# Kernel tuning notes

Measured on AMD Instinct MI355X. Metric: run time of the kernel, lower is better.

Reference implementation:

```python
import jax, jax.numpy as jnp
import numpy as np

D = 512      # input_size == per-head embed_size (wide attention)
H = 8        # num_attn_heads


def setup_inputs() -> dict:
    key = jax.random.key(0)
    ks = jax.random.split(key, 8)
    B, S = 2, 2048
    scale = 1.0 / np.sqrt(D)
    return {
        "Xin_q": jax.random.normal(ks[0], (B, S, D), dtype=jnp.float32),
        "Xin_k": jax.random.normal(ks[1], (B, S, D), dtype=jnp.float32),
        "Xin_v": jax.random.normal(ks[2], (B, S, D), dtype=jnp.float32),
        # per-head projection weights, stored as [H, D_in, D_out] (bias-free)
        "Wq": jax.random.normal(ks[3], (H, D, D), dtype=jnp.float32) * scale,
        "Wk": jax.random.normal(ks[4], (H, D, D), dtype=jnp.float32) * scale,
        "Wv": jax.random.normal(ks[5], (H, D, D), dtype=jnp.float32) * scale,
        # output projection: concat(H*D) -> D, with bias
        "Wz": jax.random.normal(ks[6], (H * D, D), dtype=jnp.float32) * (1.0 / np.sqrt(H * D)),
        "bz": jax.random.normal(ks[7], (D,), dtype=jnp.float32) * 0.01,
    }


def reference(Xin_q, Xin_k, Xin_v, Wq, Wk, Wv, Wz, bz):
    B, Sq, _ = Xin_q.shape
    inv4 = 1.0 / (D ** 0.25)  # each of Q and K scaled by embed_size**(1/4)
    # project all heads at once: [B,H,S,D]
    q = jnp.einsum("bsd,hde->bhse", Xin_q, Wq) * inv4
    k = jnp.einsum("bsd,hde->bhse", Xin_k, Wk) * inv4
    v = jnp.einsum("bsd,hde->bhse", Xin_v, Wv)
    attn = jax.nn.softmax(jnp.einsum("bhqe,bhke->bhqk", q, k), axis=-1)
    z = jnp.einsum("bhqk,bhke->bhqe", attn, v)        # [B,H,S,D]
    # concat heads along last dim (head-major order matches torch.cat over the head loop)
    z = jnp.transpose(z, (0, 2, 1, 3)).reshape(B, Sq, H * D)
    out = z @ Wz + bz                                  # [B,S,D]
    attn_avg = jnp.mean(attn, axis=1)                  # [B,Sq,Skv]
    return out, attn_avg
```

## Files before the change

### kernel.cpp

```cpp
#include <hip/hip_runtime.h>
#include <math.h>

#define BB 2
#define SS 2048
#define D_ 512
#define H_ 8
#define MS (BB * SS)
#define HD (H_ * D_)

typedef short bf16x8 __attribute__((ext_vector_type(8)));
typedef float f32x4 __attribute__((ext_vector_type(4)));

__device__ inline unsigned short f2bf(float f) {
    union { float f; unsigned u; } x{f};
    unsigned r = x.u + 0x7fff + ((x.u >> 16) & 1);
    return (unsigned short)(r >> 16);
}
__device__ inline float bf2f(unsigned short u) {
    union { unsigned u; float f; } x{(unsigned)u << 16};
    return x.f;
}

constexpr size_t SZ_X   = (size_t)MS * D_ * 2;
constexpr size_t SZ_W   = (size_t)H_ * D_ * D_ * 2;
constexpr size_t SZ_WZ  = (size_t)HD * D_ * 2;
constexpr size_t SZ_QK  = (size_t)H_ * MS * D_ * 2;
constexpr size_t SZ_SC  = (size_t)H_ * BB * SS * SS * 2;
constexpr size_t SZ_Z   = (size_t)MS * HD * 2;
constexpr size_t SZ_OP  = (size_t)2 * MS * D_ * 4;
constexpr size_t SZ_LV  = (size_t)H_ * BB * SS * 4;
constexpr size_t OFF_XQ  = 0;
constexpr size_t OFF_XK  = OFF_XQ + SZ_X;
constexpr size_t OFF_XV  = OFF_XK + SZ_X;
constexpr size_t OFF_WQT = OFF_XV + SZ_X;
constexpr size_t OFF_WKT = OFF_WQT + SZ_W;
constexpr size_t OFF_WVT = OFF_WKT + SZ_W;
constexpr size_t OFF_WZT = OFF_WVT + SZ_W;
constexpr size_t OFF_QB  = OFF_WZT + SZ_WZ;
constexpr size_t OFF_KB  = OFF_QB + SZ_QK;
constexpr size_t OFF_VT  = OFF_KB + SZ_QK;
constexpr size_t OFF_SC  = OFF_VT + SZ_QK;
constexpr size_t OFF_Z   = OFF_SC + SZ_SC;
constexpr size_t OFF_OP  = OFF_Z + SZ_Z;
constexpr size_t OFF_LV  = OFF_OP + SZ_OP;
constexpr size_t WS_TOTAL = OFF_LV + SZ_LV;
__device__ __align__(256) unsigned char g_ws[WS_TOTAL];

__device__ inline void gl2lds16(const unsigned short* g, unsigned short* l) {
    __builtin_amdgcn_global_load_lds(
        (const __attribute__((address_space(1))) void*)g,
        (__attribute__((address_space(3))) void*)l, 16, 0, 0);
}

#define BAR() __builtin_amdgcn_s_barrier()
#define PRIO1() __builtin_amdgcn_s_setprio(1)
#define PRIO0() __builtin_amdgcn_s_setprio(0)
#define VMW4() asm volatile("s_waitcnt vmcnt(4)" ::: "memory")
#define VMW0() asm volatile("s_waitcnt vmcnt(0)" ::: "memory")

__device__ __forceinline__ void rd_a(const unsigned short* p, int qm, int o0, int o1,
                                     bf16x8 (&Af)[8]) {
#pragma unroll
    for (int fi = 0; fi < 4; fi++) {
        Af[2 * fi]     = *(const bf16x8*)(p + (qm * 64 + fi * 16) * 64 + o0);
        Af[2 * fi + 1] = *(const bf16x8*)(p + (qm * 64 + fi * 16) * 64 + o1);
    }
}
__device__ __forceinline__ void rd_b(const unsigned short* p, int qn, int o0, int o1,
                                     bf16x8 (&Bf)[4]) {
#pragma unroll
    for (int fj = 0; fj < 2; fj++) {
        Bf[2 * fj]     = *(const bf16x8*)(p + (qn * 32 + fj * 16) * 64 + o0);
        Bf[2 * fj + 1] = *(const bf16x8*)(p + (qn * 32 + fj * 16) * 64 + o1);
    }
}
__device__ __forceinline__ void mma_q(int qm, int qn, const bf16x8 (&Af)[8],
                                      const bf16x8 (&Bf)[4], f32x4 (&acc)[8][4]) {
#pragma unroll
    for (int fi = 0; fi < 4; fi++)
#pragma unroll
        for (int fj = 0; fj < 2; fj++) {
            acc[qm * 4 + fi][qn * 2 + fj] = __builtin_amdgcn_mfma_f32_16x16x32_bf16(
                Af[2 * fi], Bf[2 * fj], acc[qm * 4 + fi][qn * 2 + fj], 0, 0, 0);
            acc[qm * 4 + fi][qn * 2 + fj] = __builtin_amdgcn_mfma_f32_16x16x32_bf16(
                Af[2 * fi + 1], Bf[2 * fj + 1], acc[qm * 4 + fi][qn * 2 + fj], 0, 0, 0);
        }
}

__global__ __launch_bounds__(512, 2) void gemm256_k(
    const unsigned short* __restrict__ A, const unsigned short* __restrict__ B,
    unsigned short* __restrict__ C, int K, int ldA, int ldB, int ldC,
    long sA1, long sA2, long sB1, long sB2, long sC1, long sC2, int d2,
    float alpha, int doExp, const float* __restrict__ rowScale, long sR1, long sR2,
    int gx, int gy, int gz)
{
    __shared__ unsigned short LA[2][256 * 64];
    __shared__ unsigned short LB[2][256 * 64];
    const int tid = threadIdx.x;
    const int w = tid >> 6, l = tid & 63;
    const int wm = w >> 2, wn = w & 3;

    const int sr = l >> 3;
    const int sq = (l & 7) ^ sr;
    const int q = l >> 4, sl = l & 7;
    const int o0 = (q ^ sl) * 8;
    const int o1 = ((q + 4) ^ sl) * 8;
    const unsigned short* pa0 = &LA[0][(wm * 128 + (l & 15)) * 64];
    const unsigned short* pa1 = &LA[1][(wm * 128 + (l & 15)) * 64];
    const unsigned short* pb0 = &LB[0][(wn * 64 + (l & 15)) * 64];
    const unsigned short* pb1 = &LB[1][(wn * 64 + (l & 15)) * 64];

    const int tilesPerZ = gx * gy;
    const int zPerXcd = gz >> 3;
    const int perXcd = zPerXcd * tilesPerZ;
    const int xcd = blockIdx.x & 7, jj = blockIdx.x >> 3;
    const int nT = (perXcd - jj + 31) >> 5;
    const int nK2 = K >> 7;

    auto decode = [&](int idx, const unsigned short*& gA, const unsigned short*& gB,
                      long& cO, long& rO, int& m0o, int& n0o) {
        const int zl = idx / tilesPerZ;
        const int rem = idx - zl * tilesPerZ;
        const int by = rem / gx;
        const int bx = rem - by * gx;
        const int bz = xcd * zPerXcd + zl;
        const int z1 = bz / d2, z2 = bz - z1 * d2;
        m0o = by * 256; n0o = bx * 256;
        gA = A + z1 * sA1 + z2 * sA2 + (long)(m0o + w * 16 + sr) * ldA + sq * 8;
        gB = B + z1 * sB1 + z2 * sB2 + (long)(n0o + w * 16 + sr) * ldB + sq * 8;
        cO = z1 * sC1 + z2 * sC2;
        rO = z1 * sR1 + z2 * sR2;
    };

    const unsigned short *gAc, *gBc, *gAn, *gBn;
    long cOff, rsOff, cOffN, rsOffN;
    int m0, n0, m0N, n0N;
    decode(jj, gAc, gBc, cOff, rsOff, m0, n0);
    gAn = gAc; gBn = gBc; cOffN = cOff; rsOffN = rsOff; m0N = m0; n0N = n0;

    f32x4 acc[8][4] = {};
    bf16x8 Af[8], Bf0[4], Bf1[4];

#define STG_A(bufi, half, base, t) do { \
    gl2lds16((base) + (long)((half) * 128) * ldA + (long)(t) * 64, \
             &LA[bufi][((half) * 128 + w * 16) * 64]); \
    gl2lds16((base) + (long)((half) * 128 + 8) * ldA + (long)(t) * 64, \
             &LA[bufi][((half) * 128 + w * 16 + 8) * 64]); } while (0)
#define STG_B(bufi, half, base, t) do { \
    gl2lds16((base) + (long)((half) * 128) * ldB + (long)(t) * 64, \
             &LB[bufi][((half) * 128 + w * 16) * 64]); \
    gl2lds16((base) + (long)((half) * 128 + 8) * ldB + (long)(t) * 64, \
             &LB[bufi][((half) * 128 + w * 16 + 8) * 64]); } while (0)

    STG_A(0, 0, gAc, 0); STG_A(0, 1, gAc, 0);
    STG_B(0, 0, gBc, 0); STG_B(0, 1, gBc, 0);
    STG_B(1, 0, gBc, 1); STG_B(1, 1, gBc, 1);
    VMW4();
    BAR();

    for (int k = 0; k < nT; ++k) {
        const bool hasNext = (k + 1 < nT);
        if (hasNext) decode(jj + (k + 1) * 32, gAn, gBn, cOffN, rsOffN, m0N, n0N);

        for (int u = 0; u < nK2; ++u) {
            const int t1 = 2 * u + 1, t2 = 2 * u + 2, t3 = 2 * u + 3;
            const bool lastU = (u == nK2 - 1);
            const bool stg = !lastU || hasNext;
            const unsigned short* a2 = lastU ? gAn : gAc;
            const unsigned short* b2 = lastU ? gBn : gBc;
            const int tt2 = lastU ? 0 : t2;
            const int tt3 = lastU ? 1 : t3;
            rd_a(pa0, 0, o0, o1, Af);
            rd_b(pb0, 0, o0, o1, Bf0);
            STG_A(1, 0, gAc, t1);
            BAR(); PRIO1(); mma_q(0, 0, Af, Bf0, acc); PRIO0(); BAR();
            rd_b(pb0, 1, o0, o1, Bf1);
            STG_A(1, 1, gAc, t1);
            BAR(); PRIO1(); mma_q(0, 1, Af, Bf1, acc); PRIO0(); BAR();
            rd_a(pa0, 1, o0, o1, Af);
            if (stg) STG_B(0, 0, b2, tt2);
            BAR(); PRIO1(); mma_q(1, 1, Af, Bf1, acc); PRIO0(); BAR();
            if (stg) STG_B(0, 1, b2, tt2);
            BAR(); PRIO1(); mma_q(1, 0, Af, Bf0, acc); PRIO0();
            if (stg) VMW4(); else VMW0();
            BAR();
            rd_a(pa1, 0, o0, o1, Af);
            rd_b(pb1, 0, o0, o1, Bf0);
            if (stg) STG_A(0, 0, a2, tt2);
            BAR(); PRIO1(); mma_q(0, 0, Af, Bf0, acc); PRIO0(); BAR();
            rd_b(pb1, 1, o0, o1, Bf1);
            if (stg) STG_A(0, 1, a2, tt2);
            BAR(); PRIO1(); mma_q(0, 1, Af, Bf1, acc); PRIO0(); BAR();
            rd_a(pa1, 1, o0, o1, Af);
            if (stg) STG_B(1, 0, b2, tt3);
            BAR(); PRIO1(); mma_q(1, 1, Af, Bf1, acc); PRIO0(); BAR();
            if (stg) STG_B(1, 1, b2, tt3);
            BAR(); PRIO1(); mma_q(1, 0, Af, Bf0, acc); PRIO0();
            if (stg) VMW4(); else VMW0();
            BAR();
        }

        {
            const int rowB = m0 + wm * 128 + q * 4;
            const int colB = n0 + wn * 64 + (l & 15);
            unsigned short* Cp = C + cOff;
#pragma unroll
            for (int mi = 0; mi < 8; mi++) {
#pragma unroll
                for (int rg = 0; rg < 4; rg++) {
                    const int row = rowB + mi * 16 + rg;
                    const float rs = rowScale ? rowScale[rsOff + row] : 1.0f;
#pragma unroll
                    for (int nj = 0; nj < 4; nj++) {
                        float v = alpha * acc[mi][nj][rg];
                        if (doExp) v = __expf(v);
                        Cp[(long)row * ldC + colB + nj * 16] = f2bf(v * rs);
                    }
                }
            }
        }
#pragma unroll
        for (int mi = 0; mi < 8; mi++)
#pragma unroll
            for (int nj = 0; nj < 4; nj++)
                acc[mi][nj] = (f32x4){0.f, 0.f, 0.f, 0.f};
        gAc = gAn; gBc = gBn; cOff = cOffN; rsOff = rsOffN; m0 = m0N; n0 = n0N;
    }
#undef STG_A
#undef STG_B
}

__global__ __launch_bounds__(256) void gemm_bt_k(
    const unsigned short* __restrict__ A, const unsigned short* __restrict__ B,
    void* __restrict__ Cv, int K, int ldA, int ldB, int ldC,
    long sA1, long sA2, long sB1, long sB2, long sC1, long sC2, int d2,
    float alpha, const float* __restrict__ bias, int outBf16, int doExp,
    const float* __restrict__ rowScale, long sR1, long sR2)
{
    __shared__ unsigned short As[128 * 64];
    __shared__ unsigned short Bs[128 * 64];
    const int gx = gridDim.x, gy = gridDim.y, gz = gridDim.z;
    int bx, by, bz;
    if (((gy * gz) & 7) == 0) {
        const long L = blockIdx.x + (long)gx * (blockIdx.y + (long)gy * blockIdx.z);
        const int d = (int)(L & 7);
        const long s = L >> 3;
        bx = (int)(s % gx);
        const long yz = d + 8 * (s / gx);
        by = (int)(yz % gy);
        bz = (int)(yz / gy);
    } else {
        bx = blockIdx.x; by = blockIdx.y; bz = blockIdx.z;
    }
    const int z1 = bz / d2, z2 = bz % d2;
    A += z1 * sA1 + z2 * sA2;
    B += z1 * sB1 + z2 * sB2;
    const long cOff = z1 * sC1 + z2 * sC2;
    const long rsOff = z1 * sR1 + z2 * sR2;
    const int m0 = by * 128, n0 = bx * 128;
    const int tid = threadIdx.x;
    const int w = tid >> 6, l = tid & 63;

    const int sr = l >> 3;
    const int sq = (l & 7) ^ sr;
    const unsigned short* ga = A + (long)(m0 + w * 32 + sr) * ldA + sq * 8;
    const unsigned short* gb = B + (long)(n0 + w * 32 + sr) * ldB + sq * 8;
    unsigned short* laA = As + w * 2048;
    unsigned short* laB = Bs + w * 2048;

    const int wm = w >> 1, wn = w & 1;
    const int q = l >> 4;
    const int sl = l & 7;
    const int mA = wm * 64 + (l & 15);
    const int nB = wn * 64 + (l & 15);
    const int s0 = ((q) ^ sl) * 8;
    const int s1 = ((q + 4) ^ sl) * 8;
    const unsigned short* pa0 = As + mA * 64 + s0;
    const unsigned short* pa1 = As + mA * 64 + s1;
    const unsigned short* pb0 = Bs + nB * 64 + s0;
    const unsigned short* pb1 = Bs + nB * 64 + s1;

    f32x4 acc[4][4] = {};
    for (int kk = 0; kk < K; kk += 64) {
#pragma unroll
        for (int i = 0; i < 4; i++) {
            gl2lds16(ga + (long)i * 8 * ldA, laA + i * 512);
            gl2lds16(gb + (long)i * 8 * ldB, laB + i * 512);
        }
        ga += 64; gb += 64;
        __syncthreads();
        bf16x8 af[4], bf[4];
#pragma unroll
        for (int i = 0; i < 4; i++) {
            af[i] = *(const bf16x8*)(pa0 + i * 1024);
            bf[i] = *(const bf16x8*)(pb0 + i * 1024);
        }
#pragma unroll
        for (int mi = 0; mi < 4; mi++)
#pragma unroll
            for (int ni = 0; ni < 4; ni++)
                acc[mi][ni] = __builtin_amdgcn_mfma_f32_16x16x32_bf16(
                    af[mi], bf[ni], acc[mi][ni], 0, 0, 0);
#pragma unroll
        for (int i = 0; i < 4; i++) {
            af[i] = *(const bf16x8*)(pa1 + i * 1024);
            bf[i] = *(const bf16x8*)(pb1 + i * 1024);
        }
#pragma unroll
        for (int mi = 0; mi < 4; mi++)
#pragma unroll
            for (int ni = 0; ni < 4; ni++)
                acc[mi][ni] = __builtin_amdgcn_mfma_f32_16x16x32_bf16(
                    af[mi], bf[ni], acc[mi][ni], 0, 0, 0);
        __syncthreads();
    }

    const int rowB = m0 + wm * 64 + q * 4;
    const int colB = n0 + wn * 64 + (l & 15);
    if (outBf16) {
        unsigned short* C = (unsigned short*)Cv + cOff;
#pragma unroll
        for (int mi = 0; mi < 4; mi++) {
#pragma unroll
            for (int rg = 0; rg < 4; rg++) {
                const int row = rowB + mi * 16 + rg;
                const float rs = rowScale ? rowScale[rsOff + row] : 1.0f;
#pragma unroll
                for (int ni = 0; ni < 4; ni++) {
                    float v = alpha * acc[mi][ni][rg];
                    if (doExp) v = __expf(v);
                    C[(long)row * ldC + colB + ni * 16] = f2bf(v * rs);
                }
            }
        }
    } else {
        float* C = (float*)Cv + cOff;
#pragma unroll
        for (int ni = 0; ni < 4; ni++) {
            const int col = colB + ni * 16;
            const float bs = bias ? bias[col] : 0.f;
#pragma unroll
            for (int mi = 0; mi < 4; mi++)
#pragma unroll
                for (int rg = 0; rg < 4; rg++)
                    C[(long)(rowB + mi * 16 + rg) * ldC + col] =
                        alpha * acc[mi][ni][rg] + bs;
        }
    }
}

__global__ __launch_bounds__(256) void cvt3_k(
    const float* __restrict__ i0, const float* __restrict__ i1, const float* __restrict__ i2,
    unsigned short* __restrict__ o0, unsigned short* __restrict__ o1,
    unsigned short* __restrict__ o2, long n4)
{
    const float* in = blockIdx.z == 0 ? i0 : (blockIdx.z == 1 ? i1 : i2);
    unsigned short* out = blockIdx.z == 0 ? o0 : (blockIdx.z == 1 ? o1 : o2);
    long i = (long)blockIdx.x * 256 + threadIdx.x;
    if (i >= n4) return;
    float4 v = ((const float4*)in)[i];
    ushort4 o;
    o.x = f2bf(v.x); o.y = f2bf(v.y); o.z = f2bf(v.z); o.w = f2bf(v.w);
    ((ushort4*)out)[i] = o;
}

__global__ __launch_bounds__(256) void transcvt3_k(
    const float* __restrict__ i0, const float* __restrict__ i1, const float* __restrict__ i2,
    unsigned short* __restrict__ o0, unsigned short* __restrict__ o1,
    unsigned short* __restrict__ o2)
{
    __shared__ float t[32][33];
    const int zt = blockIdx.z >> 3, h = blockIdx.z & 7;
    const float* in = (zt == 0 ? i0 : (zt == 1 ? i1 : i2)) + (long)h * D_ * D_;
    unsigned short* out = (zt == 0 ? o0 : (zt == 1 ? o1 : o2)) + (long)h * D_ * D_;
    const int r0 = blockIdx.y * 32, c0 = blockIdx.x * 32;
    const int tr = threadIdx.x >> 5, tc = threadIdx.x & 31;
#pragma unroll
    for (int i = 0; i < 4; i++)
        t[tr + i * 8][tc] = in[(long)(r0 + tr + i * 8) * D_ + c0 + tc];
    __syncthreads();
#pragma unroll
    for (int i = 0; i < 4; i++)
        out[(long)(c0 + tr + i * 8) * D_ + r0 + tc] = f2bf(t[tc][tr + i * 8]);
}

__global__ __launch_bounds__(256) void transcvt_k(
    const float* __restrict__ in, unsigned short* __restrict__ out, int R, int C)
{
    __shared__ float t[32][33];
    const int r0 = blockIdx.y * 32, c0 = blockIdx.x * 32;
    const int tr = threadIdx.x >> 5, tc = threadIdx.x & 31;
#pragma unroll
    for (int i = 0; i < 4; i++)
        t[tr + i * 8][tc] = in[(long)(r0 + tr + i * 8) * C + c0 + tc];
    __syncthreads();
#pragma unroll
    for (int i = 0; i < 4; i++)
        out[(long)(c0 + tr + i * 8) * R + r0 + tc] = f2bf(t[tc][tr + i * 8]);
}

__device__ inline float wred_sum(float v) {
#pragma unroll
    for (int o = 32; o; o >>= 1) v += __shfl_down(v, o);
    return v;
}
__global__ __launch_bounds__(256) void sumavg_k(
    const unsigned short* __restrict__ E, float* __restrict__ avg,
    float* __restrict__ linv)
{
    const int blk = blockIdx.x;
    const int b = blk >> 11, s = blk & (SS - 1);
    const int tid = threadIdx.x;
    __shared__ float red[4];
    float av[8] = {};
    const int t0 = tid * 8;
    for (int h = 0; h < H_; h++) {
        const long rowOff = ((long)(h * BB + b) * SS + s) * SS + t0;
        const ushort4 u0 = *(const ushort4*)(E + rowOff);
        const ushort4 u1 = *(const ushort4*)(E + rowOff + 4);
        float vals[8] = {bf2f(u0.x), bf2f(u0.y), bf2f(u0.z), bf2f(u0.w),
                         bf2f(u1.x), bf2f(u1.y), bf2f(u1.z), bf2f(u1.w)};
        float sum = 0.f;
#pragma unroll
        for (int i = 0; i < 8; i++) sum += vals[i];
        float wsum = wred_sum(sum);
        if ((tid & 63) == 0) red[tid >> 6] = wsum;
        __syncthreads();
        sum = red[0] + red[1] + red[2] + red[3];
        __syncthreads();
        const float inv = 1.0f / sum;
        if (tid == 0) linv[(long)(h * BB + b) * SS + s] = inv;
        const float invH = inv * 0.125f;
#pragma unroll
        for (int i = 0; i < 8; i++) av[i] += vals[i] * invH;
    }
    const long aOff = ((long)b * SS + s) * SS + t0;
    float4 a0 = {av[0], av[1], av[2], av[3]};
    float4 a1 = {av[4], av[5], av[6], av[7]};
    *(float4*)(avg + aOff) = a0;
    *(float4*)(avg + aOff + 4) = a1;
}

__global__ __launch_bounds__(256) void addbias_k(
    const float* __restrict__ p0, const float* __restrict__ p1,
    const float* __restrict__ bz, float* __restrict__ out)
{
    const long n4 = (long)MS * D_ / 4;
    long i = (long)blockIdx.x * 256 + threadIdx.x;
    if (i >= n4) return;
    const int col4 = (int)((i * 4) & (D_ - 1));
    float4 a = ((const float4*)p0)[i];
    float4 b = ((const float4*)p1)[i];
    float4 c = *(const float4*)(bz + col4);
    float4 o = {a.x + b.x + c.x, a.y + b.y + c.y, a.z + b.z + c.z, a.w + b.w + c.w};
    ((float4*)out)[i] = o;
}

extern "C" void kernel_launch(void* const* d_in, const int* in_sizes, int n_in,
                              void* d_out, int out_size, void* d_ws, size_t ws_size,
                              hipStream_t stream)
{
    const float* Xq = (const float*)d_in[0];
    const float* Xk = (const float*)d_in[1];
    const float* Xv = (const float*)d_in[2];
    const float* Wq = (const float*)d_in[3];
    const float* Wk = (const float*)d_in[4];
    const float* Wv = (const float*)d_in[5];
    const float* Wz = (const float*)d_in[6];
    const float* bz = (const float*)d_in[7];

    float* out      = (float*)d_out;
    float* attn_avg = out + (long)MS * D_;

    unsigned char* ws = nullptr;
    (void)hipGetSymbolAddress((void**)&ws, HIP_SYMBOL(g_ws));
    unsigned short* Xbq = (unsigned short*)(ws + OFF_XQ);
    unsigned short* Xbk = (unsigned short*)(ws + OFF_XK);
    unsigned short* Xbv = (unsigned short*)(ws + OFF_XV);
    unsigned short* Wqt = (unsigned short*)(ws + OFF_WQT);
    unsigned short* Wkt = (unsigned short*)(ws + OFF_WKT);
    unsigned short* Wvt = (unsigned short*)(ws + OFF_WVT);
    unsigned short* Wzt = (unsigned short*)(ws + OFF_WZT);
    unsigned short* qb  = (unsigned short*)(ws + OFF_QB);
    unsigned short* vT  = (unsigned short*)(ws + OFF_VT);
    unsigned short* scb = (unsigned short*)(ws + OFF_SC);
    unsigned short* zal = (unsigned short*)(ws + OFF_Z);
    float*          opp = (float*)(ws + OFF_OP);
    float*          linv = (float*)(ws + OFF_LV);

    const float inv4 = 1.0f / powf((float)D_, 0.25f);

    const long n4x = (long)MS * D_ / 4;
    cvt3_k<<<dim3((n4x + 255) / 256, 1, 3), 256, 0, stream>>>(
        Xq, Xk, Xv, Xbq, Xbk, Xbv, n4x);
    transcvt3_k<<<dim3(16, 16, 24), 256, 0, stream>>>(Wq, Wk, Wv, Wqt, Wkt, Wvt);
    transcvt_k<<<dim3(16, 128, 1), 256, 0, stream>>>(Wz, Wzt, HD, D_);

    gemm256_k<<<dim3(256), 512, 0, stream>>>(
        Xbq, Wqt, qb, D_, D_, D_, D_,
        (long)MS * D_, 0, (long)H_ * D_ * D_, (long)D_ * D_,
        (long)H_ * MS * D_, (long)MS * D_, 8, inv4, 0, nullptr, 0, 0,
        2, 16, 16);
    gemm256_k<<<dim3(256), 512, 0, stream>>>(
        Wvt, Xbv, vT, D_, D_, D_, SS,
        (long)D_ * D_, 0, 0, (long)SS * D_, (long)2 * D_ * SS, (long)D_ * SS, 2,
        1.0f, 0, nullptr, 0, 0,
        8, 2, 16);

    gemm256_k<<<dim3(256), 512, 0, stream>>>(
        qb, qb + (long)H_ * MS * D_, scb, D_, D_, D_, SS,
        (long)MS * D_, (long)SS * D_, (long)MS * D_, (long)SS * D_,
        (long)2 * SS * SS, (long)SS * SS, 2, 1.0f, 1, nullptr, 0, 0,
        8, 8, 16);

    sumavg_k<<<dim3(BB * SS), 256, 0, stream>>>(scb, attn_avg, linv);

    gemm256_k<<<dim3(256), 512, 0, stream>>>(
        scb, vT, zal, SS, SS, SS, HD,
        (long)2 * SS * SS, (long)SS * SS, (long)2 * D_ * SS, (long)D_ * SS,
        512, (long)SS * HD, 2, 1.0f, 0,
        linv, (long)BB * SS, (long)SS,
        2, 8, 16);

    gemm_bt_k<<<dim3(4, 32, 2), 256, 0, stream>>>(
        zal, Wzt, opp, HD / 2, HD, HD, D_,
        0, 2048, 0, 2048, 0, (long)MS * D_, 2, 1.0f, nullptr, 0, 0, nullptr, 0, 0);
    const long n4o = (long)MS * D_ / 4;
    addbias_k<<<dim3((n4o + 255) / 256), 256, 0, stream>>>(
        opp, opp + (long)MS * D_, bz, out);
}
```

Measured before the change: 457.3 us.

## Permute B-tile column mapping so epilogue writes four contiguous bf16 outputs

Changes how B rows are assigned to MFMA lanes so each lane owns four adjacent output columns instead of columns strided by 16. This lets the epilogue pack four bf16 results into one 8-byte store rather than four 2-byte scattered stores. To keep LDS reads conflict-free, the global-to-LDS staging for B uses two separate base pointers with a new XOR swizzle. The risk is that the new swizzle causes bank conflicts or an indexing mismatch that yields wrong results.

```diff
diff --git a/kernel.cpp b/kernel.cpp
--- a/kernel.cpp
+++ b/kernel.cpp
@@ -70,8 +70,9 @@
                                      bf16x8 (&Bf)[4]) {
 #pragma unroll
     for (int fj = 0; fj < 2; fj++) {
-        Bf[2 * fj]     = *(const bf16x8*)(p + (qn * 32 + fj * 16) * 64 + o0);
-        Bf[2 * fj + 1] = *(const bf16x8*)(p + (qn * 32 + fj * 16) * 64 + o1);
+        const int t = qn * 2 + fj;
+        Bf[2 * fj]     = *(const bf16x8*)(p + t * 64 + o0);
+        Bf[2 * fj + 1] = *(const bf16x8*)(p + t * 64 + o1);
     }
 }
 __device__ __forceinline__ void mma_q(int qm, int qn, const bf16x8 (&Af)[8],
@@ -101,14 +102,16 @@
     const int wm = w >> 2, wn = w & 3;
 
     const int sr = l >> 3;
-    const int sq = (l & 7) ^ sr;
+    const int sqA = (l & 7) ^ sr;
+    const int sqB0 = (l & 7) ^ ((w * 4 + (sr >> 2)) & 7);
+    const int sqB1 = sqB0 ^ 2;
     const int q = l >> 4, sl = l & 7;
     const int o0 = (q ^ sl) * 8;
     const int o1 = ((q + 4) ^ sl) * 8;
     const unsigned short* pa0 = &LA[0][(wm * 128 + (l & 15)) * 64];
     const unsigned short* pa1 = &LA[1][(wm * 128 + (l & 15)) * 64];
-    const unsigned short* pb0 = &LB[0][(wn * 64 + (l & 15)) * 64];
-    const unsigned short* pb1 = &LB[1][(wn * 64 + (l & 15)) * 64];
+    const unsigned short* pb0 = &LB[0][(wn * 64 + (l & 15) * 4) * 64];
+    const unsigned short* pb1 = &LB[1][(wn * 64 + (l & 15) * 4) * 64];
 
     const int tilesPerZ = gx * gy;
     const int zPerXcd = gz >> 3;
@@ -117,7 +120,8 @@
     const int nT = (perXcd - jj + 31) >> 5;
     const int nK2 = K >> 7;
 
-    auto decode = [&](int idx, const unsigned short*& gA, const unsigned short*& gB,
+    auto decode = [&](int idx, const unsigned short*& gA,
+                      const unsigned short*& gB0, const unsigned short*& gB1,
                       long& cO, long& rO, int& m0o, int& n0o) {
         const int zl = idx / tilesPerZ;
         const int rem = idx - zl * tilesPerZ;
@@ -126,17 +130,21 @@
         const int bz = xcd * zPerXcd + zl;
         const int z1 = bz / d2, z2 = bz - z1 * d2;
         m0o = by * 256; n0o = bx * 256;
-        gA = A + z1 * sA1 + z2 * sA2 + (long)(m0o + w * 16 + sr) * ldA + sq * 8;
-        gB = B + z1 * sB1 + z2 * sB2 + (long)(n0o + w * 16 + sr) * ldB + sq * 8;
+        const unsigned short* Az = A + z1 * sA1 + z2 * sA2;
+        const unsigned short* Bz = B + z1 * sB1 + z2 * sB2;
+        gA  = Az + (long)(m0o + w * 16 + sr) * ldA + sqA * 8;
+        gB0 = Bz + (long)(n0o + w * 16 + sr) * ldB + sqB0 * 8;
+        gB1 = Bz + (long)(n0o + w * 16 + 8 + sr) * ldB + sqB1 * 8;
         cO = z1 * sC1 + z2 * sC2;
         rO = z1 * sR1 + z2 * sR2;
     };
 
-    const unsigned short *gAc, *gBc, *gAn, *gBn;
+    const unsigned short *gAc, *gB0c, *gB1c, *gAn, *gB0n, *gB1n;
     long cOff, rsOff, cOffN, rsOffN;
     int m0, n0, m0N, n0N;
-    decode(jj, gAc, gBc, cOff, rsOff, m0, n0);
-    gAn = gAc; gBn = gBc; cOffN = cOff; rsOffN = rsOff; m0N = m0; n0N = n0;
+    decode(jj, gAc, gB0c, gB1c, cOff, rsOff, m0, n0);
+    gAn = gAc; gB0n = gB0c; gB1n = gB1c;
+    cOffN = cOff; rsOffN = rsOff; m0N = m0; n0N = n0;
 
     f32x4 acc[8][4] = {};
     bf16x8 Af[8], Bf0[4], Bf1[4];
@@ -146,28 +154,30 @@
              &LA[bufi][((half) * 128 + w * 16) * 64]); \
     gl2lds16((base) + (long)((half) * 128 + 8) * ldA + (long)(t) * 64, \
              &LA[bufi][((half) * 128 + w * 16 + 8) * 64]); } while (0)
-#define STG_B(bufi, half, base, t) do { \
-    gl2lds16((base) + (long)((half) * 128) * ldB + (long)(t) * 64, \
+#define STG_B(bufi, half, b0, b1, t) do { \
+    gl2lds16((b0) + (long)((half) * 128) * ldB + (long)(t) * 64, \
              &LB[bufi][((half) * 128 + w * 16) * 64]); \
-    gl2lds16((base) + (long)((half) * 128 + 8) * ldB + (long)(t) * 64, \
+    gl2lds16((b1) + (long)((half) * 128) * ldB + (long)(t) * 64, \
              &LB[bufi][((half) * 128 + w * 16 + 8) * 64]); } while (0)
 
     STG_A(0, 0, gAc, 0); STG_A(0, 1, gAc, 0);
-    STG_B(0, 0, gBc, 0); STG_B(0, 1, gBc, 0);
-    STG_B(1, 0, gBc, 1); STG_B(1, 1, gBc, 1);
+    STG_B(0, 0, gB0c, gB1c, 0); STG_B(0, 1, gB0c, gB1c, 0);
+    STG_B(1, 0, gB0c, gB1c, 1); STG_B(1, 1, gB0c, gB1c, 1);
     VMW4();
     BAR();
 
     for (int k = 0; k < nT; ++k) {
         const bool hasNext = (k + 1 < nT);
-        if (hasNext) decode(jj + (k + 1) * 32, gAn, gBn, cOffN, rsOffN, m0N, n0N);
+        if (hasNext) decode(jj + (k + 1) * 32, gAn, gB0n, gB1n,
+                            cOffN, rsOffN, m0N, n0N);
 
         for (int u = 0; u < nK2; ++u) {
             const int t1 = 2 * u + 1, t2 = 2 * u + 2, t3 = 2 * u + 3;
             const bool lastU = (u == nK2 - 1);
             const bool stg = !lastU || hasNext;
             const unsigned short* a2 = lastU ? gAn : gAc;
-            const unsigned short* b2 = lastU ? gBn : gBc;
+            const unsigned short* b20 = lastU ? gB0n : gB0c;
+            const unsigned short* b21 = lastU ? gB1n : gB1c;
             const int tt2 = lastU ? 0 : t2;
             const int tt3 = lastU ? 1 : t3;
             rd_a(pa0, 0, o0, o1, Af);
@@ -178,9 +188,9 @@
             STG_A(1, 1, gAc, t1);
             BAR(); PRIO1(); mma_q(0, 1, Af, Bf1, acc); PRIO0(); BAR();
             rd_a(pa0, 1, o0, o1, Af);
-            if (stg) STG_B(0, 0, b2, tt2);
+            if (stg) STG_B(0, 0, b20, b21, tt2);
             BAR(); PRIO1(); mma_q(1, 1, Af, Bf1, acc); PRIO0(); BAR();
-            if (stg) STG_B(0, 1, b2, tt2);
+            if (stg) STG_B(0, 1, b20, b21, tt2);
             BAR(); PRIO1(); mma_q(1, 0, Af, Bf0, acc); PRIO0();
             if (stg) VMW4(); else VMW0();
             BAR();
@@ -192,9 +202,9 @@
             if (stg) STG_A(0, 1, a2, tt2);
             BAR(); PRIO1(); mma_q(0, 1, Af, Bf1, acc); PRIO0(); BAR();
             rd_a(pa1, 1, o0, o1, Af);
-            if (stg) STG_B(1, 0, b2, tt3);
+            if (stg) STG_B(1, 0, b20, b21, tt3);
             BAR(); PRIO1(); mma_q(1, 1, Af, Bf1, acc); PRIO0(); BAR();
-            if (stg) STG_B(1, 1, b2, tt3);
+            if (stg) STG_B(1, 1, b20, b21, tt3);
             BAR(); PRIO1(); mma_q(1, 0, Af, Bf0, acc); PRIO0();
             if (stg) VMW4(); else VMW0();
             BAR();
@@ -202,7 +212,7 @@
 
         {
             const int rowB = m0 + wm * 128 + q * 4;
-            const int colB = n0 + wn * 64 + (l & 15);
+            const int colB = n0 + wn * 64 + (l & 15) * 4;
             unsigned short* Cp = C + cOff;
 #pragma unroll
             for (int mi = 0; mi < 8; mi++) {
@@ -210,12 +220,18 @@
                 for (int rg = 0; rg < 4; rg++) {
                     const int row = rowB + mi * 16 + rg;
                     const float rs = rowScale ? rowScale[rsOff + row] : 1.0f;
-#pragma unroll
-                    for (int nj = 0; nj < 4; nj++) {
-                        float v = alpha * acc[mi][nj][rg];
-                        if (doExp) v = __expf(v);
-                        Cp[(long)row * ldC + colB + nj * 16] = f2bf(v * rs);
+                    float v0 = alpha * acc[mi][0][rg];
+                    float v1 = alpha * acc[mi][1][rg];
+                    float v2 = alpha * acc[mi][2][rg];
+                    float v3 = alpha * acc[mi][3][rg];
+                    if (doExp) {
+                        v0 = __expf(v0); v1 = __expf(v1);
+                        v2 = __expf(v2); v3 = __expf(v3);
                     }
+                    uint2 pk;
+                    pk.x = (unsigned)f2bf(v0 * rs) | ((unsigned)f2bf(v1 * rs) << 16);
+                    pk.y = (unsigned)f2bf(v2 * rs) | ((unsigned)f2bf(v3 * rs) << 16);
+                    *(uint2*)(Cp + (long)row * ldC + colB) = pk;
                 }
             }
         }
@@ -224,7 +240,8 @@
 #pragma unroll
             for (int nj = 0; nj < 4; nj++)
                 acc[mi][nj] = (f32x4){0.f, 0.f, 0.f, 0.f};
-        gAc = gAn; gBc = gBn; cOff = cOffN; rsOff = rsOffN; m0 = m0N; n0 = n0N;
+        gAc = gAn; gB0c = gB0n; gB1c = gB1n;
+        cOff = cOffN; rsOff = rsOffN; m0 = m0N; n0 = n0N;
     }
 #undef STG_A
 #undef STG_B
```

After: 451.6 us. About the same (-1.2%).
